# Kernel optimization log

Measured on AMD Instinct MI355X. Metric: run time of the kernel, lower is better.

Reference implementation:

```python
import jax, jax.numpy as jnp
import numpy as np

EPS = 1e-3  # keras BatchNormalization default epsilon


def _dwconv_t(y, w):
    # depthwise conv along time (axis 1), SAME padding. y:(B,T,S,G,n), w:(G,n,k)
    k = w.shape[-1]
    T = y.shape[1]
    pl = (k - 1) // 2
    yp = jnp.pad(y, ((0, 0), (pl, k - 1 - pl), (0, 0), (0, 0), (0, 0)))
    return sum(yp[:, j:j + T] * w[..., j] for j in range(k))


def _tc_layer(x, w, b, k3, k5, k7, gamma, beta, mu, var):
    # x:(B,T,S,C); w:(5,G,Cg,nb); b/gamma/beta/mu/var:(5,G,nb); k*:(G,nb,k)
    B, T, S, C = x.shape
    G, nb = w.shape[1], w.shape[-1]
    # global spatial pooling: concat [x, max, mean] along spatial axis -> S+2
    x = jnp.concatenate([x, x.max(axis=2, keepdims=True), x.mean(axis=2, keepdims=True)], axis=2)
    S = S + 2
    xg = x.reshape(B, T, S, G, C // G)
    # 5 grouped 1x1x1 pointwise convs at once
    y = jnp.einsum('btsgc,pgcn->pbtsgn', xg, w) + b[:, None, None, None]
    t0 = y[0]
    t3 = _dwconv_t(y[1], k3)
    t5 = _dwconv_t(y[2], k5)
    t7 = _dwconv_t(y[3], k7)
    # temporal maxpool pool=2 stride=1 SAME (TF pads right)
    t1 = jnp.maximum(y[4], jnp.concatenate([y[4][:, 1:], y[4][:, -1:]], axis=1))
    ts = jnp.stack([t0, t3, t5, t7, t1])  # (5,B,T,S,G,nb)
    scale = gamma[:, None, None, None] / jnp.sqrt(var[:, None, None, None] + EPS)
    ts = (ts - mu[:, None, None, None]) * scale + beta[:, None, None, None]
    # concat branches within each group: (B,T,S,G,5*nb)
    z = jnp.transpose(ts, (1, 2, 3, 4, 0, 5)).reshape(B, T, S, G, 5 * nb)
    z = jax.nn.relu(z)
    # channel shuffle: (G, per) -> (per, G) -> flatten
    z = jnp.swapaxes(z, -1, -2).reshape(B, T, S, G * 5 * nb)
    # MaxPooling3D pool=(2,1,1) stride 2 valid: halve T
    return jnp.maximum(z[:, 0::2], z[:, 1::2])


def setup_inputs() -> dict:
    key = jax.random.key(0)
    ks = jax.random.split(key, 32)
    B, T, H, W, C = 16, 64, 7, 7, 1024
    G = 8
    d = {'x': jax.random.normal(ks[0], (B, T, H, W, C), jnp.float32)}
    specs = [(0, 128, 32), (1, 160, 40)]  # (layer, Cg, nb)
    i = 1
    for l, cg, nb in specs:
        d[f'w{l}'] = 0.02 * jax.random.normal(ks[i], (5, G, cg, nb)); i += 1
        d[f'b{l}'] = 0.02 * jax.random.normal(ks[i], (5, G, nb)); i += 1
        d[f'k3_{l}'] = 0.1 * jax.random.normal(ks[i], (G, nb, 3)); i += 1
        d[f'k5_{l}'] = 0.1 * jax.random.normal(ks[i], (G, nb, 5)); i += 1
        d[f'k7_{l}'] = 0.1 * jax.random.normal(ks[i], (G, nb, 7)); i += 1
        d[f'g{l}'] = jax.random.uniform(ks[i], (5, G, nb), minval=0.5, maxval=1.5); i += 1
        d[f'be{l}'] = 0.02 * jax.random.normal(ks[i], (5, G, nb)); i += 1
        d[f'mu{l}'] = 0.02 * jax.random.normal(ks[i], (5, G, nb)); i += 1
        d[f'v{l}'] = jax.random.uniform(ks[i], (5, G, nb), minval=0.5, maxval=1.5); i += 1
    return d


def reference(x, w0, b0, k3_0, k5_0, k7_0, g0, be0, mu0, v0,
              w1, b1, k3_1, k5_1, k7_1, g1, be1, mu1, v1):
    B, T, H, W, C = x.shape
    z = x.reshape(B, T, H * W, C)  # (B,T,S,C), side_dim2=1 kept implicit
    z = _tc_layer(z, w0, b0, k3_0, k5_0, k7_0, g0, be0, mu0, v0)
    z = _tc_layer(z, w1, b1, k3_1, k5_1, k7_1, g1, be1, mu1, v1)
    return z[:, :, :, None, :]  # (B, T/4, S+4, 1, Cout)
```

## Files before the change

kernel.cpp:

```cpp
#include <hip/hip_runtime.h>
#include <hip/hip_bf16.h>

#define EPSBN 1e-3f

typedef __attribute__((ext_vector_type(8))) short bf16x8;
typedef __attribute__((ext_vector_type(8))) unsigned short ushort8;
typedef __attribute__((ext_vector_type(4))) float f32x4;


__device__ __forceinline__ float bf2f(unsigned short u) {
    union { unsigned int i; float f; } c; c.i = (unsigned int)u << 16; return c.f;
}
__device__ __forceinline__ unsigned short f2bf(float f) {
    union { float f; unsigned int i; } c; c.f = f;
    unsigned int r = c.i + 0x7FFF + ((c.i >> 16) & 1);
    return (unsigned short)(r >> 16);
}

__global__ __launch_bounds__(256) void tc_prep(const float* __restrict__ w0,
                                               const float* __restrict__ w1,
                                               unsigned short* __restrict__ W0t,
                                               unsigned short* __restrict__ W1t) {
    const int idx = blockIdx.x * 256 + threadIdx.x;
    if (idx < 163840) {
        const int g   = idx / 20480;
        const int rem = idx - g*20480;
        const int n   = rem >> 7;
        const int k   = rem & 127;
        const int p   = n >> 5, nn = n & 31;
        W0t[idx] = f2bf(w0[(((size_t)p*8 + g)*128 + k)*32 + nn]);
    } else if (idx < 163840 + 256000) {
        const int i2  = idx - 163840;
        const int g   = i2 / 32000;
        const int rem = i2 - g*32000;
        const int n   = rem / 160;
        const int k   = rem - n*160;
        const int kref = (k % 20)*8 + k/20;
        const int p   = n / 40, nn = n - p*40;
        W1t[i2] = f2bf(w1[(((size_t)p*8 + g)*160 + kref)*40 + nn]);
    }
}

__global__ __launch_bounds__(256) void tc_reduce0(const float* __restrict__ x,
                                                  unsigned short* __restrict__ xb,
                                                  unsigned short* __restrict__ extb,
                                                  const int big) {
    const int bt = blockIdx.x;
    const int b  = bt >> 6, t = bt & 63;
    const int c  = threadIdx.x * 4;
    const float4* src = reinterpret_cast<const float4*>(x + (size_t)bt * 49 * 1024 + c);
    float4 v = src[0];
    float mx0 = v.x, mx1 = v.y, mx2 = v.z, mx3 = v.w;
    float sm0 = v.x, sm1 = v.y, sm2 = v.z, sm3 = v.w;
    if (big) {
        ushort4 o; o.x=f2bf(v.x); o.y=f2bf(v.y); o.z=f2bf(v.z); o.w=f2bf(v.w);
        *reinterpret_cast<ushort4*>(&xb[((size_t)(b*51)*64 + t)*1024 + c]) = o;
    }
    for (int s = 1; s < 49; ++s) {
        float4 u = src[(size_t)s * 256];
        mx0 = fmaxf(mx0, u.x); sm0 += u.x;
        mx1 = fmaxf(mx1, u.y); sm1 += u.y;
        mx2 = fmaxf(mx2, u.z); sm2 += u.z;
        mx3 = fmaxf(mx3, u.w); sm3 += u.w;
        if (big) {
            ushort4 o; o.x=f2bf(u.x); o.y=f2bf(u.y); o.z=f2bf(u.z); o.w=f2bf(u.w);
            *reinterpret_cast<ushort4*>(&xb[((size_t)(b*51 + s)*64 + t)*1024 + c]) = o;
        }
    }
    const float inv = 1.0f / 49.0f;
    ushort4 omx, omn;
    omx.x=f2bf(mx0); omx.y=f2bf(mx1); omx.z=f2bf(mx2); omx.w=f2bf(mx3);
    omn.x=f2bf(sm0*inv); omn.y=f2bf(sm1*inv); omn.z=f2bf(sm2*inv); omn.w=f2bf(sm3*inv);
    if (big) {
        *reinterpret_cast<ushort4*>(&xb[((size_t)(b*51 + 49)*64 + t)*1024 + c]) = omx;
        *reinterpret_cast<ushort4*>(&xb[((size_t)(b*51 + 50)*64 + t)*1024 + c]) = omn;
    } else {
        *reinterpret_cast<ushort4*>(&extb[((size_t)(b*2 + 0)*64 + t)*1024 + c]) = omx;
        *reinterpret_cast<ushort4*>(&extb[((size_t)(b*2 + 1)*64 + t)*1024 + c]) = omn;
    }
}

template<int BIG>
__global__ __launch_bounds__(256, 5) void tc_layer0(
    const float* __restrict__ x, const unsigned short* __restrict__ xb,
    const unsigned short* __restrict__ extb,
    const unsigned short* __restrict__ W0t, const float* __restrict__ bias,
    const float* __restrict__ k3, const float* __restrict__ k5,
    const float* __restrict__ k7,
    const float* __restrict__ gam, const float* __restrict__ bet,
    const float* __restrict__ mu, const float* __restrict__ var,
    unsigned short* __restrict__ zb)
{
    const int tid = threadIdx.x;
    const int g  = blockIdx.x / 816;
    const int bs = blockIdx.x % 816;
    const int s  = bs % 51;
    const int b  = bs / 51;

    __shared__ __align__(16) unsigned short lds[15104];
    unsigned short* AtU = lds;
    unsigned short* WtU = lds + 64*136;
    unsigned short* Ytb = lds;

    #pragma unroll
    for (int it = 0; it < 4; ++it) {
        const int fid = tid + it*256;
        const int row = fid >> 4;
        const int ch8 = (fid & 15) * 8;
        ushort8 u;
        if (BIG) {
            u = *reinterpret_cast<const ushort8*>(
                &xb[((size_t)(b*51 + s)*64 + row)*1024 + g*128 + ch8]);
        } else if (s < 49) {
            const float* sp = x + ((size_t)(b*64 + row)*49 + s)*1024 + g*128 + ch8;
            const float4 f0 = *reinterpret_cast<const float4*>(sp);
            const float4 f1 = *reinterpret_cast<const float4*>(sp + 4);
            u[0]=f2bf(f0.x); u[1]=f2bf(f0.y); u[2]=f2bf(f0.z); u[3]=f2bf(f0.w);
            u[4]=f2bf(f1.x); u[5]=f2bf(f1.y); u[6]=f2bf(f1.z); u[7]=f2bf(f1.w);
        } else {
            u = *reinterpret_cast<const ushort8*>(
                &extb[((size_t)(b*2 + (s-49))*64 + row)*1024 + g*128 + ch8]);
        }
        *reinterpret_cast<ushort8*>(&AtU[row*136 + ch8]) = u;
    }

    const int lane = tid & 63;
    const int wid  = tid >> 6;
    const int fr   = lane & 15;
    const int kb   = lane >> 4;

    f32x4 zero = {0.f, 0.f, 0.f, 0.f};
    f32x4 acc[10];
    #pragma unroll
    for (int i = 0; i < 10; ++i) acc[i] = zero;

    for (int kc = 0; kc < 4; ++kc) {
        __syncthreads();
        #pragma unroll
        for (int it = 0; it < 3; ++it) {
            const int gi = tid + it*256;
            if (gi < 640) {
                const int n = gi >> 2, part = (gi & 3) * 8;
                *reinterpret_cast<ushort8*>(&WtU[n*40 + part]) =
                    *reinterpret_cast<const ushort8*>(
                        &W0t[((size_t)g*160 + n)*128 + kc*32 + part]);
            }
        }
        __syncthreads();
        const bf16x8 bfrag = *reinterpret_cast<const bf16x8*>(
            &AtU[(wid*16 + fr)*136 + kc*32 + kb*8]);
        #pragma unroll
        for (int nt = 0; nt < 10; ++nt) {
            const bf16x8 afrag = *reinterpret_cast<const bf16x8*>(
                &WtU[(nt*16 + fr)*40 + kb*8]);
            acc[nt] = __builtin_amdgcn_mfma_f32_16x16x32_bf16(afrag, bfrag, acc[nt], 0, 0, 0);
        }
    }
    __syncthreads();
    #pragma unroll
    for (int nt = 0; nt < 10; ++nt)
        #pragma unroll
        for (int r = 0; r < 4; ++r)
            Ytb[(nt*16 + kb*4 + r)*72 + wid*16 + fr] = f2bf(acc[nt][r]);
    __syncthreads();

    if (tid < 160) {
        const int ch = tid;
        const int p  = ch >> 5, n = ch & 31;
        const int pi = (p*8 + g)*32 + n;
        const float bsv = bias[pi];
        const float sc  = gam[pi]*rsqrtf(var[pi]+EPSBN);
        const float sh  = bet[pi] - mu[pi]*sc;
        float yv[64];
        #pragma unroll
        for (int i = 0; i < 8; ++i) {
            const ushort8 u = *reinterpret_cast<const ushort8*>(&Ytb[ch*72 + i*8]);
            #pragma unroll
            for (int j = 0; j < 8; ++j) yv[i*8+j] = bf2f(u[j]) + bsv;
        }
        unsigned short* zp = zb + ((size_t)(b*32)*53 + s)*1280 + g*160 + ch;
        if (p == 0) {
            #pragma unroll
            for (int tq = 0; tq < 32; ++tq) {
                const float r = fmaxf(fmaxf(fmaf(yv[2*tq],sc,sh), fmaf(yv[2*tq+1],sc,sh)), 0.f);
                zp[(size_t)tq*67840] = f2bf(r);
            }
        } else if (p == 1) {
            const float w0_ = k3[(g*32+n)*3+0], w1_ = k3[(g*32+n)*3+1], w2_ = k3[(g*32+n)*3+2];
            #pragma unroll
            for (int tq = 0; tq < 32; ++tq) {
                float a = yv[2*tq]*w1_;
                if (tq > 0) a = fmaf(yv[2*tq-1], w0_, a);
                a = fmaf(yv[2*tq+1], w2_, a);
                float c2 = fmaf(yv[2*tq], w0_, yv[2*tq+1]*w1_);
                if (tq < 31) c2 = fmaf(yv[2*tq+2], w2_, c2);
                const float r = fmaxf(fmaxf(fmaf(a,sc,sh), fmaf(c2,sc,sh)), 0.f);
                zp[(size_t)tq*67840] = f2bf(r);
            }
        } else if (p == 2) {
            float wk[5];
            #pragma unroll
            for (int j = 0; j < 5; ++j) wk[j] = k5[(g*32+n)*5+j];
            #pragma unroll
            for (int tq = 0; tq < 32; ++tq) {
                float vv[2];
                #pragma unroll
                for (int q = 0; q < 2; ++q) {
                    const int t = 2*tq + q;
                    float v = 0.f;
                    #pragma unroll
                    for (int j = 0; j < 5; ++j) {
                        const int ttp = t + j - 2;
                        if (ttp >= 0 && ttp < 64) v = fmaf(yv[ttp], wk[j], v);
                    }
                    vv[q] = v;
                }
                const float r = fmaxf(fmaxf(fmaf(vv[0],sc,sh), fmaf(vv[1],sc,sh)), 0.f);
                zp[(size_t)tq*67840] = f2bf(r);
            }
        } else if (p == 3) {
            float wk[7];
            #pragma unroll
            for (int j = 0; j < 7; ++j) wk[j] = k7[(g*32+n)*7+j];
            #pragma unroll
            for (int tq = 0; tq < 32; ++tq) {
                float vv[2];
                #pragma unroll
                for (int q = 0; q < 2; ++q) {
                    const int t = 2*tq + q;
                    float v = 0.f;
                    #pragma unroll
                    for (int j = 0; j < 7; ++j) {
                        const int ttp = t + j - 3;
                        if (ttp >= 0 && ttp < 64) v = fmaf(yv[ttp], wk[j], v);
                    }
                    vv[q] = v;
                }
                const float r = fmaxf(fmaxf(fmaf(vv[0],sc,sh), fmaf(vv[1],sc,sh)), 0.f);
                zp[(size_t)tq*67840] = f2bf(r);
            }
        } else {
            #pragma unroll
            for (int tq = 0; tq < 32; ++tq) {
                const float v0 = fmaxf(yv[2*tq], yv[2*tq+1]);
                const float v1 = fmaxf(yv[2*tq+1], yv[(2*tq+2 < 64) ? 2*tq+2 : 63]);
                const float r = fmaxf(fmaxf(fmaf(v0,sc,sh), fmaf(v1,sc,sh)), 0.f);
                zp[(size_t)tq*67840] = f2bf(r);
            }
        }
    }
}

__global__ __launch_bounds__(320) void tc_reduce1(unsigned short* __restrict__ zb) {
    const int bt = blockIdx.x;
    const int c  = threadIdx.x * 4;
    unsigned short* base = zb + (size_t)bt * 67840;
    ushort4 u = *reinterpret_cast<const ushort4*>(&base[c]);
    float v0 = bf2f(u.x), v1 = bf2f(u.y), v2 = bf2f(u.z), v3 = bf2f(u.w);
    float mx0 = v0, mx1 = v1, mx2 = v2, mx3 = v3;
    float sm0 = v0, sm1 = v1, sm2 = v2, sm3 = v3;
    for (int s = 1; s < 51; ++s) {
        ushort4 w = *reinterpret_cast<const ushort4*>(&base[(size_t)s*1280 + c]);
        v0 = bf2f(w.x); v1 = bf2f(w.y); v2 = bf2f(w.z); v3 = bf2f(w.w);
        mx0 = fmaxf(mx0, v0); sm0 += v0;
        mx1 = fmaxf(mx1, v1); sm1 += v1;
        mx2 = fmaxf(mx2, v2); sm2 += v2;
        mx3 = fmaxf(mx3, v3); sm3 += v3;
    }
    const float inv = 1.0f / 51.0f;
    ushort4 o;
    o.x = f2bf(mx0); o.y = f2bf(mx1); o.z = f2bf(mx2); o.w = f2bf(mx3);
    *reinterpret_cast<ushort4*>(&base[(size_t)51*1280 + c]) = o;
    o.x = f2bf(sm0*inv); o.y = f2bf(sm1*inv); o.z = f2bf(sm2*inv); o.w = f2bf(sm3*inv);
    *reinterpret_cast<ushort4*>(&base[(size_t)52*1280 + c]) = o;
}

__global__ __launch_bounds__(256, 6) void tc_layer1(
    const unsigned short* __restrict__ zbi,
    const unsigned short* __restrict__ W1t, const float* __restrict__ bias,
    const float* __restrict__ k3, const float* __restrict__ k5,
    const float* __restrict__ k7,
    const float* __restrict__ gam, const float* __restrict__ bet,
    const float* __restrict__ mu, const float* __restrict__ var,
    float* __restrict__ out)
{
    const int tid = threadIdx.x;
    const int g  = blockIdx.x / 848;
    const int bs = blockIdx.x % 848;
    const int s  = bs % 53;
    const int b  = bs / 53;

    __shared__ __align__(16) unsigned short lds[13376];
    unsigned short* AtU = lds;
    unsigned short* WtU = lds + 32*168;
    unsigned short* Ytb = lds;

    #pragma unroll
    for (int it = 0; it < 5; ++it) {
        const int fid = tid + it*256;
        const int t   = fid / 40;
        const int seg = fid - t*40;
        const int gg  = seg / 5, q = seg - gg*5;
        const int ch  = gg*160 + g*20 + q*4;
        const unsigned short* src = zbi + ((size_t)(b*32 + t)*53 + s)*1280 + ch;
        *reinterpret_cast<ushort4*>(&AtU[t*168 + seg*4]) =
            *reinterpret_cast<const ushort4*>(src);
    }

    const int lane = tid & 63;
    const int wid  = tid >> 6;
    const int tt_  = wid & 1;
    const int nh   = wid >> 1;
    const int nbase = nh * 7;
    const int fr   = lane & 15;
    const int kb   = lane >> 4;

    f32x4 zero = {0.f, 0.f, 0.f, 0.f};
    f32x4 acc[7];
    #pragma unroll
    for (int i = 0; i < 7; ++i) acc[i] = zero;

    for (int kc = 0; kc < 5; ++kc) {
        __syncthreads();
        #pragma unroll
        for (int it = 0; it < 4; ++it) {
            const int gi = tid + it*256;
            if (gi < 800) {
                const int n = gi >> 2, part = (gi & 3) * 8;
                *reinterpret_cast<ushort8*>(&WtU[n*40 + part]) =
                    *reinterpret_cast<const ushort8*>(
                        &W1t[((size_t)g*200 + n)*160 + kc*32 + part]);
            }
        }
        __syncthreads();
        const bf16x8 bfrag = *reinterpret_cast<const bf16x8*>(
            &AtU[(tt_*16 + fr)*168 + kc*32 + kb*8]);
        #pragma unroll
        for (int i = 0; i < 7; ++i) {
            const int nt = nbase + i;
            if (nt < 13) {
                const bf16x8 afrag = *reinterpret_cast<const bf16x8*>(
                    &WtU[(nt*16 + fr)*40 + kb*8]);
                acc[i] = __builtin_amdgcn_mfma_f32_16x16x32_bf16(afrag, bfrag, acc[i], 0, 0, 0);
            }
        }
    }
    __syncthreads();
    #pragma unroll
    for (int i = 0; i < 7; ++i) {
        const int nt = nbase + i;
        if (nt < 13) {
            #pragma unroll
            for (int r = 0; r < 4; ++r) {
                const int row = nt*16 + kb*4 + r;
                if (row < 200) Ytb[row*40 + tt_*16 + fr] = f2bf(acc[i][r]);
            }
        }
    }
    __syncthreads();

    if (tid < 200) {
        const int ch = tid;
        const int p  = ch / 40, n = ch - p*40;
        const int pi = (p*8 + g)*40 + n;
        const float bsv = bias[pi];
        const float sc  = gam[pi]*rsqrtf(var[pi]+EPSBN);
        const float sh  = bet[pi] - mu[pi]*sc;
        float yv[32];
        #pragma unroll
        for (int i = 0; i < 4; ++i) {
            const ushort8 u = *reinterpret_cast<const ushort8*>(&Ytb[ch*40 + i*8]);
            #pragma unroll
            for (int j = 0; j < 8; ++j) yv[i*8+j] = bf2f(u[j]) + bsv;
        }
        float* op = out + ((size_t)(b*16)*53 + s)*1600 + g*200 + ch;
        if (p == 0) {
            #pragma unroll
            for (int tq = 0; tq < 16; ++tq)
                op[(size_t)tq*84800] =
                    fmaxf(fmaxf(fmaf(yv[2*tq],sc,sh), fmaf(yv[2*tq+1],sc,sh)), 0.f);
        } else if (p == 1) {
            const float w0_ = k3[(g*40+n)*3+0], w1_ = k3[(g*40+n)*3+1], w2_ = k3[(g*40+n)*3+2];
            #pragma unroll
            for (int tq = 0; tq < 16; ++tq) {
                float a = yv[2*tq]*w1_;
                if (tq > 0) a = fmaf(yv[2*tq-1], w0_, a);
                a = fmaf(yv[2*tq+1], w2_, a);
                float c2 = fmaf(yv[2*tq], w0_, yv[2*tq+1]*w1_);
                if (tq < 15) c2 = fmaf(yv[2*tq+2], w2_, c2);
                op[(size_t)tq*84800] = fmaxf(fmaxf(fmaf(a,sc,sh), fmaf(c2,sc,sh)), 0.f);
            }
        } else if (p == 2) {
            float wk[5];
            #pragma unroll
            for (int j = 0; j < 5; ++j) wk[j] = k5[(g*40+n)*5+j];
            #pragma unroll
            for (int tq = 0; tq < 16; ++tq) {
                float vv[2];
                #pragma unroll
                for (int q = 0; q < 2; ++q) {
                    const int t = 2*tq + q;
                    float v = 0.f;
                    #pragma unroll
                    for (int j = 0; j < 5; ++j) {
                        const int ttp = t + j - 2;
                        if (ttp >= 0 && ttp < 32) v = fmaf(yv[ttp], wk[j], v);
                    }
                    vv[q] = v;
                }
                op[(size_t)tq*84800] = fmaxf(fmaxf(fmaf(vv[0],sc,sh), fmaf(vv[1],sc,sh)), 0.f);
            }
        } else if (p == 3) {
            float wk[7];
            #pragma unroll
            for (int j = 0; j < 7; ++j) wk[j] = k7[(g*40+n)*7+j];
            #pragma unroll
            for (int tq = 0; tq < 16; ++tq) {
                float vv[2];
                #pragma unroll
                for (int q = 0; q < 2; ++q) {
                    const int t = 2*tq + q;
                    float v = 0.f;
                    #pragma unroll
                    for (int j = 0; j < 7; ++j) {
                        const int ttp = t + j - 3;
                        if (ttp >= 0 && ttp < 32) v = fmaf(yv[ttp], wk[j], v);
                    }
                    vv[q] = v;
                }
                op[(size_t)tq*84800] = fmaxf(fmaxf(fmaf(vv[0],sc,sh), fmaf(vv[1],sc,sh)), 0.f);
            }
        } else {
            #pragma unroll
            for (int tq = 0; tq < 16; ++tq) {
                const float v0 = fmaxf(yv[2*tq], yv[2*tq+1]);
                const float v1 = fmaxf(yv[2*tq+1], yv[(2*tq+2 < 32) ? 2*tq+2 : 31]);
                op[(size_t)tq*84800] = fmaxf(fmaxf(fmaf(v0,sc,sh), fmaf(v1,sc,sh)), 0.f);
            }
        }
    }
}

__global__ __launch_bounds__(256) void tc_shuffle(float* __restrict__ o) {
    __shared__ float row[1600];
    const size_t base = (size_t)blockIdx.x * 1600;
    const int tid = threadIdx.x;
    #pragma unroll
    for (int it = 0; it < 2; ++it) {
        const int f4 = tid + it*256;
        if (f4 < 400)
            *reinterpret_cast<float4*>(&row[f4*4]) =
                *reinterpret_cast<const float4*>(&o[base + (size_t)f4*4]);
    }
    __syncthreads();
    #pragma unroll
    for (int it = 0; it < 2; ++it) {
        const int f4 = tid + it*256;
        if (f4 < 400) {
            const int c = f4*4;
            float4 v;
            v.x = row[((c  ) & 7)*200 + ((c  ) >> 3)];
            v.y = row[((c+1) & 7)*200 + ((c+1) >> 3)];
            v.z = row[((c+2) & 7)*200 + ((c+2) >> 3)];
            v.w = row[((c+3) & 7)*200 + ((c+3) >> 3)];
            *reinterpret_cast<float4*>(&o[base + (size_t)c]) = v;
        }
    }
}

extern "C" void kernel_launch(void* const* d_in, const int* in_sizes, int n_in,
                              void* d_out, int out_size, void* d_ws, size_t ws_size,
                              hipStream_t stream) {
    const float* x    = (const float*)d_in[0];
    const float* w0   = (const float*)d_in[1];
    const float* b0   = (const float*)d_in[2];
    const float* k3_0 = (const float*)d_in[3];
    const float* k5_0 = (const float*)d_in[4];
    const float* k7_0 = (const float*)d_in[5];
    const float* g0   = (const float*)d_in[6];
    const float* be0  = (const float*)d_in[7];
    const float* mu0  = (const float*)d_in[8];
    const float* v0   = (const float*)d_in[9];
    const float* w1   = (const float*)d_in[10];
    const float* b1   = (const float*)d_in[11];
    const float* k3_1 = (const float*)d_in[12];
    const float* k5_1 = (const float*)d_in[13];
    const float* k7_1 = (const float*)d_in[14];
    const float* g1   = (const float*)d_in[15];
    const float* be1  = (const float*)d_in[16];
    const float* mu1  = (const float*)d_in[17];
    const float* v1   = (const float*)d_in[18];

    const size_t n_zb   = 34734080;
    const size_t n_W0t  = 163840;
    const size_t n_W1t  = 256000;
    const size_t n_extb = 2097152;
    const size_t n_xb   = 53477376;

    unsigned short* zb   = (unsigned short*)d_ws;
    unsigned short* W0t  = zb + n_zb;
    unsigned short* W1t  = W0t + n_W0t;
    unsigned short* extb = W1t + n_W1t;
    unsigned short* xb   = extb + n_extb;
    const size_t need_big = (n_zb + n_W0t + n_W1t + n_extb + n_xb) * 2;
    const int big = (ws_size >= need_big) ? 1 : 0;

    tc_prep   <<<1640, 256, 0, stream>>>(w0, w1, W0t, W1t);
    tc_reduce0<<<16*64, 256, 0, stream>>>(x, xb, extb, big);
    if (big)
        tc_layer0<1><<<816*8, 256, 0, stream>>>(x, xb, extb, W0t, b0, k3_0, k5_0,
                                                k7_0, g0, be0, mu0, v0, zb);
    else
        tc_layer0<0><<<816*8, 256, 0, stream>>>(x, xb, extb, W0t, b0, k3_0, k5_0,
                                                k7_0, g0, be0, mu0, v0, zb);
    tc_reduce1<<<16*32, 320, 0, stream>>>(zb);
    tc_layer1 <<<848*8, 256, 0, stream>>>(zb, W1t, b1, k3_1, k5_1, k7_1,
                                          g1, be1, mu1, v1, (float*)d_out);
    tc_shuffle<<<16*16*53, 256, 0, stream>>>((float*)d_out);
}
```

Measured before the change: 286.6 us.

## Process two spatial positions per layer1 block and stage output in bf16

Layer1 blocks now cover two spatial positions, 64 time rows, so each block loads its weight tiles once for twice the work, with each wave computing all 13 N-tiles. The layer1 intermediate is written as bf16 to a new workspace buffer and converted to fp32 in the shuffle kernel, which halves scatter-write and reread traffic. The LDS row stride drops from 72 to 70 in layer0 and is 70 in layer1, read with 32-bit loads, to reduce bank conflicts. The cost is more accumulator registers, lower occupancy (launch bound 4), an extra bf16 rounding of the output, and a larger workspace requirement.

```diff
diff --git a/kernel.cpp b/kernel.cpp
--- a/kernel.cpp
+++ b/kernel.cpp
@@ -161,7 +161,7 @@
     for (int nt = 0; nt < 10; ++nt)
         #pragma unroll
         for (int r = 0; r < 4; ++r)
-            Ytb[(nt*16 + kb*4 + r)*72 + wid*16 + fr] = f2bf(acc[nt][r]);
+            Ytb[(nt*16 + kb*4 + r)*70 + wid*16 + fr] = f2bf(acc[nt][r]);
     __syncthreads();
 
     if (tid < 160) {
@@ -173,10 +173,10 @@
         const float sh  = bet[pi] - mu[pi]*sc;
         float yv[64];
         #pragma unroll
-        for (int i = 0; i < 8; ++i) {
-            const ushort8 u = *reinterpret_cast<const ushort8*>(&Ytb[ch*72 + i*8]);
-            #pragma unroll
-            for (int j = 0; j < 8; ++j) yv[i*8+j] = bf2f(u[j]) + bsv;
+        for (int i = 0; i < 32; ++i) {
+            const unsigned int w2 = *reinterpret_cast<const unsigned int*>(&Ytb[ch*70 + i*2]);
+            yv[2*i]   = bf2f((unsigned short)(w2 & 0xffffu)) + bsv;
+            yv[2*i+1] = bf2f((unsigned short)(w2 >> 16)) + bsv;
         }
         unsigned short* zp = zb + ((size_t)(b*32)*53 + s)*1280 + g*160 + ch;
         if (p == 0) {
@@ -275,50 +275,57 @@
     *reinterpret_cast<ushort4*>(&base[(size_t)52*1280 + c]) = o;
 }
 
-__global__ __launch_bounds__(256, 6) void tc_layer1(
+__global__ __launch_bounds__(256, 4) void tc_layer1(
     const unsigned short* __restrict__ zbi,
     const unsigned short* __restrict__ W1t, const float* __restrict__ bias,
     const float* __restrict__ k3, const float* __restrict__ k5,
     const float* __restrict__ k7,
     const float* __restrict__ gam, const float* __restrict__ bet,
     const float* __restrict__ mu, const float* __restrict__ var,
-    float* __restrict__ out)
+    unsigned short* __restrict__ og)
 {
     const int tid = threadIdx.x;
-    const int g  = blockIdx.x / 848;
-    const int bs = blockIdx.x % 848;
-    const int s  = bs % 53;
-    const int b  = bs / 53;
-
-    __shared__ __align__(16) unsigned short lds[13376];
+    const int g   = blockIdx.x / 432;
+    const int rem = blockIdx.x % 432;
+    const int sp  = rem % 27;
+    const int b   = rem / 27;
+    const int s0  = sp*2;
+    const int has1 = (s0 + 1 < 53);
+
+    __shared__ __align__(16) unsigned short lds[64*168 + 208*40];
     unsigned short* AtU = lds;
-    unsigned short* WtU = lds + 32*168;
+    unsigned short* WtU = lds + 64*168;
     unsigned short* Ytb = lds;
 
-    #pragma unroll
-    for (int it = 0; it < 5; ++it) {
+    if (tid < 40) {
+        ushort8 z8 = {0,0,0,0,0,0,0,0};
+        const int r = tid / 5, cp = tid - r*5;
+        *reinterpret_cast<ushort8*>(&WtU[(200 + r)*40 + cp*8]) = z8;
+    }
+
+    #pragma unroll
+    for (int it = 0; it < 10; ++it) {
         const int fid = tid + it*256;
-        const int t   = fid / 40;
-        const int seg = fid - t*40;
+        const int row = fid / 40;
+        const int seg = fid - row*40;
         const int gg  = seg / 5, q = seg - gg*5;
         const int ch  = gg*160 + g*20 + q*4;
+        const int s   = (row < 32) ? s0 : (has1 ? s0+1 : s0);
+        const int t   = row & 31;
         const unsigned short* src = zbi + ((size_t)(b*32 + t)*53 + s)*1280 + ch;
-        *reinterpret_cast<ushort4*>(&AtU[t*168 + seg*4]) =
+        *reinterpret_cast<ushort4*>(&AtU[row*168 + seg*4]) =
             *reinterpret_cast<const ushort4*>(src);
     }
 
     const int lane = tid & 63;
     const int wid  = tid >> 6;
-    const int tt_  = wid & 1;
-    const int nh   = wid >> 1;
-    const int nbase = nh * 7;
     const int fr   = lane & 15;
     const int kb   = lane >> 4;
 
     f32x4 zero = {0.f, 0.f, 0.f, 0.f};
-    f32x4 acc[7];
-    #pragma unroll
-    for (int i = 0; i < 7; ++i) acc[i] = zero;
+    f32x4 acc[13];
+    #pragma unroll
+    for (int i = 0; i < 13; ++i) acc[i] = zero;
 
     for (int kc = 0; kc < 5; ++kc) {
         __syncthreads();
@@ -334,124 +341,128 @@
         }
         __syncthreads();
         const bf16x8 bfrag = *reinterpret_cast<const bf16x8*>(
-            &AtU[(tt_*16 + fr)*168 + kc*32 + kb*8]);
-        #pragma unroll
-        for (int i = 0; i < 7; ++i) {
-            const int nt = nbase + i;
-            if (nt < 13) {
-                const bf16x8 afrag = *reinterpret_cast<const bf16x8*>(
-                    &WtU[(nt*16 + fr)*40 + kb*8]);
-                acc[i] = __builtin_amdgcn_mfma_f32_16x16x32_bf16(afrag, bfrag, acc[i], 0, 0, 0);
-            }
+            &AtU[(wid*16 + fr)*168 + kc*32 + kb*8]);
+        #pragma unroll
+        for (int nt = 0; nt < 13; ++nt) {
+            const bf16x8 afrag = *reinterpret_cast<const bf16x8*>(
+                &WtU[(nt*16 + fr)*40 + kb*8]);
+            acc[nt] = __builtin_amdgcn_mfma_f32_16x16x32_bf16(afrag, bfrag, acc[nt], 0, 0, 0);
         }
     }
     __syncthreads();
     #pragma unroll
-    for (int i = 0; i < 7; ++i) {
-        const int nt = nbase + i;
-        if (nt < 13) {
-            #pragma unroll
-            for (int r = 0; r < 4; ++r) {
-                const int row = nt*16 + kb*4 + r;
-                if (row < 200) Ytb[row*40 + tt_*16 + fr] = f2bf(acc[i][r]);
-            }
+    for (int nt = 0; nt < 13; ++nt) {
+        #pragma unroll
+        for (int r = 0; r < 4; ++r) {
+            const int n = nt*16 + kb*4 + r;
+            if (n < 200) Ytb[n*70 + wid*16 + fr] = f2bf(acc[nt][r]);
         }
     }
     __syncthreads();
 
-    if (tid < 200) {
-        const int ch = tid;
-        const int p  = ch / 40, n = ch - p*40;
-        const int pi = (p*8 + g)*40 + n;
-        const float bsv = bias[pi];
-        const float sc  = gam[pi]*rsqrtf(var[pi]+EPSBN);
-        const float sh  = bet[pi] - mu[pi]*sc;
-        float yv[32];
-        #pragma unroll
-        for (int i = 0; i < 4; ++i) {
-            const ushort8 u = *reinterpret_cast<const ushort8*>(&Ytb[ch*40 + i*8]);
-            #pragma unroll
-            for (int j = 0; j < 8; ++j) yv[i*8+j] = bf2f(u[j]) + bsv;
-        }
-        float* op = out + ((size_t)(b*16)*53 + s)*1600 + g*200 + ch;
-        if (p == 0) {
-            #pragma unroll
-            for (int tq = 0; tq < 16; ++tq)
-                op[(size_t)tq*84800] =
-                    fmaxf(fmaxf(fmaf(yv[2*tq],sc,sh), fmaf(yv[2*tq+1],sc,sh)), 0.f);
-        } else if (p == 1) {
-            const float w0_ = k3[(g*40+n)*3+0], w1_ = k3[(g*40+n)*3+1], w2_ = k3[(g*40+n)*3+2];
-            #pragma unroll
-            for (int tq = 0; tq < 16; ++tq) {
-                float a = yv[2*tq]*w1_;
-                if (tq > 0) a = fmaf(yv[2*tq-1], w0_, a);
-                a = fmaf(yv[2*tq+1], w2_, a);
-                float c2 = fmaf(yv[2*tq], w0_, yv[2*tq+1]*w1_);
-                if (tq < 15) c2 = fmaf(yv[2*tq+2], w2_, c2);
-                op[(size_t)tq*84800] = fmaxf(fmaxf(fmaf(a,sc,sh), fmaf(c2,sc,sh)), 0.f);
-            }
-        } else if (p == 2) {
-            float wk[5];
-            #pragma unroll
-            for (int j = 0; j < 5; ++j) wk[j] = k5[(g*40+n)*5+j];
-            #pragma unroll
-            for (int tq = 0; tq < 16; ++tq) {
-                float vv[2];
-                #pragma unroll
-                for (int q = 0; q < 2; ++q) {
-                    const int t = 2*tq + q;
-                    float v = 0.f;
+    #pragma unroll
+    for (int it = 0; it < 2; ++it) {
+        const int task = tid + it*256;
+        if (task < 400) {
+            const int sIdx = (task >= 200) ? 1 : 0;
+            const int ch   = task - sIdx*200;
+            if (sIdx && !has1) continue;
+            const int s  = s0 + sIdx;
+            const int p  = ch / 40, n = ch - p*40;
+            const int pi = (p*8 + g)*40 + n;
+            const float bsv = bias[pi];
+            const float sc  = gam[pi]*rsqrtf(var[pi]+EPSBN);
+            const float sh  = bet[pi] - mu[pi]*sc;
+            float yv[32];
+            #pragma unroll
+            for (int i = 0; i < 16; ++i) {
+                const unsigned int w2 = *reinterpret_cast<const unsigned int*>(
+                    &Ytb[ch*70 + sIdx*32 + i*2]);
+                yv[2*i]   = bf2f((unsigned short)(w2 & 0xffffu)) + bsv;
+                yv[2*i+1] = bf2f((unsigned short)(w2 >> 16)) + bsv;
+            }
+            unsigned short* op = og + ((size_t)(b*16)*53 + s)*1600 + g*200 + ch;
+            if (p == 0) {
+                #pragma unroll
+                for (int tq = 0; tq < 16; ++tq) {
+                    const float r = fmaxf(fmaxf(fmaf(yv[2*tq],sc,sh), fmaf(yv[2*tq+1],sc,sh)), 0.f);
+                    op[(size_t)tq*84800] = f2bf(r);
+                }
+            } else if (p == 1) {
+                const float w0_ = k3[(g*40+n)*3+0], w1_ = k3[(g*40+n)*3+1], w2_ = k3[(g*40+n)*3+2];
+                #pragma unroll
+                for (int tq = 0; tq < 16; ++tq) {
+                    float a = yv[2*tq]*w1_;
+                    if (tq > 0) a = fmaf(yv[2*tq-1], w0_, a);
+                    a = fmaf(yv[2*tq+1], w2_, a);
+                    float c2 = fmaf(yv[2*tq], w0_, yv[2*tq+1]*w1_);
+                    if (tq < 15) c2 = fmaf(yv[2*tq+2], w2_, c2);
+                    const float r = fmaxf(fmaxf(fmaf(a,sc,sh), fmaf(c2,sc,sh)), 0.f);
+                    op[(size_t)tq*84800] = f2bf(r);
+                }
+            } else if (p == 2) {
+                float wk[5];
+                #pragma unroll
+                for (int j = 0; j < 5; ++j) wk[j] = k5[(g*40+n)*5+j];
+                #pragma unroll
+                for (int tq = 0; tq < 16; ++tq) {
+                    float vv[2];
                     #pragma unroll
-                    for (int j = 0; j < 5; ++j) {
-                        const int ttp = t + j - 2;
-                        if (ttp >= 0 && ttp < 32) v = fmaf(yv[ttp], wk[j], v);
+                    for (int q = 0; q < 2; ++q) {
+                        const int t = 2*tq + q;
+                        float v = 0.f;
+                        #pragma unroll
+                        for (int j = 0; j < 5; ++j) {
+                            const int ttp = t + j - 2;
+                            if (ttp >= 0 && ttp < 32) v = fmaf(yv[ttp], wk[j], v);
+                        }
+                        vv[q] = v;
                     }
-                    vv[q] = v;
-                }
-                op[(size_t)tq*84800] = fmaxf(fmaxf(fmaf(vv[0],sc,sh), fmaf(vv[1],sc,sh)), 0.f);
-            }
-        } else if (p == 3) {
-            float wk[7];
-            #pragma unroll
-            for (int j = 0; j < 7; ++j) wk[j] = k7[(g*40+n)*7+j];
-            #pragma unroll
-            for (int tq = 0; tq < 16; ++tq) {
-                float vv[2];
-                #pragma unroll
-                for (int q = 0; q < 2; ++q) {
-                    const int t = 2*tq + q;
-                    float v = 0.f;
+                    const float r = fmaxf(fmaxf(fmaf(vv[0],sc,sh), fmaf(vv[1],sc,sh)), 0.f);
+                    op[(size_t)tq*84800] = f2bf(r);
+                }
+            } else if (p == 3) {
+                float wk[7];
+                #pragma unroll
+                for (int j = 0; j < 7; ++j) wk[j] = k7[(g*40+n)*7+j];
+                #pragma unroll
+                for (int tq = 0; tq < 16; ++tq) {
+                    float vv[2];
                     #pragma unroll
-                    for (int j = 0; j < 7; ++j) {
-                        const int ttp = t + j - 3;
-                        if (ttp >= 0 && ttp < 32) v = fmaf(yv[ttp], wk[j], v);
+                    for (int q = 0; q < 2; ++q) {
+                        const int t = 2*tq + q;
+                        float v = 0.f;
+                        #pragma unroll
+                        for (int j = 0; j < 7; ++j) {
+                            const int ttp = t + j - 3;
+                            if (ttp >= 0 && ttp < 32) v = fmaf(yv[ttp], wk[j], v);
+                        }
+                        vv[q] = v;
                     }
-                    vv[q] = v;
-                }
-                op[(size_t)tq*84800] = fmaxf(fmaxf(fmaf(vv[0],sc,sh), fmaf(vv[1],sc,sh)), 0.f);
-            }
-        } else {
-            #pragma unroll
-            for (int tq = 0; tq < 16; ++tq) {
-                const float v0 = fmaxf(yv[2*tq], yv[2*tq+1]);
-                const float v1 = fmaxf(yv[2*tq+1], yv[(2*tq+2 < 32) ? 2*tq+2 : 31]);
-                op[(size_t)tq*84800] = fmaxf(fmaxf(fmaf(v0,sc,sh), fmaf(v1,sc,sh)), 0.f);
-            }
-        }
-    }
-}
-
-__global__ __launch_bounds__(256) void tc_shuffle(float* __restrict__ o) {
-    __shared__ float row[1600];
+                    const float r = fmaxf(fmaxf(fmaf(vv[0],sc,sh), fmaf(vv[1],sc,sh)), 0.f);
+                    op[(size_t)tq*84800] = f2bf(r);
+                }
+            } else {
+                #pragma unroll
+                for (int tq = 0; tq < 16; ++tq) {
+                    const float v0 = fmaxf(yv[2*tq], yv[2*tq+1]);
+                    const float v1 = fmaxf(yv[2*tq+1], yv[(2*tq+2 < 32) ? 2*tq+2 : 31]);
+                    const float r = fmaxf(fmaxf(fmaf(v0,sc,sh), fmaf(v1,sc,sh)), 0.f);
+                    op[(size_t)tq*84800] = f2bf(r);
+                }
+            }
+        }
+    }
+}
+
+__global__ __launch_bounds__(256) void tc_shuffle(const unsigned short* __restrict__ og,
+                                                  float* __restrict__ o) {
+    __shared__ unsigned short row[1600];
     const size_t base = (size_t)blockIdx.x * 1600;
     const int tid = threadIdx.x;
-    #pragma unroll
-    for (int it = 0; it < 2; ++it) {
-        const int f4 = tid + it*256;
-        if (f4 < 400)
-            *reinterpret_cast<float4*>(&row[f4*4]) =
-                *reinterpret_cast<const float4*>(&o[base + (size_t)f4*4]);
-    }
+    if (tid < 200)
+        *reinterpret_cast<ushort8*>(&row[tid*8]) =
+            *reinterpret_cast<const ushort8*>(&og[base + (size_t)tid*8]);
     __syncthreads();
     #pragma unroll
     for (int it = 0; it < 2; ++it) {
@@ -459,10 +470,10 @@
         if (f4 < 400) {
             const int c = f4*4;
             float4 v;
-            v.x = row[((c  ) & 7)*200 + ((c  ) >> 3)];
-            v.y = row[((c+1) & 7)*200 + ((c+1) >> 3)];
-            v.z = row[((c+2) & 7)*200 + ((c+2) >> 3)];
-            v.w = row[((c+3) & 7)*200 + ((c+3) >> 3)];
+            v.x = bf2f(row[((c  ) & 7)*200 + ((c  ) >> 3)]);
+            v.y = bf2f(row[((c+1) & 7)*200 + ((c+1) >> 3)]);
+            v.z = bf2f(row[((c+2) & 7)*200 + ((c+2) >> 3)]);
+            v.w = bf2f(row[((c+3) & 7)*200 + ((c+3) >> 3)]);
             *reinterpret_cast<float4*>(&o[base + (size_t)c]) = v;
         }
     }
@@ -495,14 +506,16 @@
     const size_t n_W0t  = 163840;
     const size_t n_W1t  = 256000;
     const size_t n_extb = 2097152;
+    const size_t n_og   = 21708800;
     const size_t n_xb   = 53477376;
 
     unsigned short* zb   = (unsigned short*)d_ws;
     unsigned short* W0t  = zb + n_zb;
     unsigned short* W1t  = W0t + n_W0t;
     unsigned short* extb = W1t + n_W1t;
-    unsigned short* xb   = extb + n_extb;
-    const size_t need_big = (n_zb + n_W0t + n_W1t + n_extb + n_xb) * 2;
+    unsigned short* og   = extb + n_extb;
+    unsigned short* xb   = og + n_og;
+    const size_t need_big = (n_zb + n_W0t + n_W1t + n_extb + n_og + n_xb) * 2;
     const int big = (ws_size >= need_big) ? 1 : 0;
 
     tc_prep   <<<1640, 256, 0, stream>>>(w0, w1, W0t, W1t);
@@ -514,7 +527,7 @@
         tc_layer0<0><<<816*8, 256, 0, stream>>>(x, xb, extb, W0t, b0, k3_0, k5_0,
                                                 k7_0, g0, be0, mu0, v0, zb);
     tc_reduce1<<<16*32, 320, 0, stream>>>(zb);
-    tc_layer1 <<<848*8, 256, 0, stream>>>(zb, W1t, b1, k3_1, k5_1, k7_1,
-                                          g1, be1, mu1, v1, (float*)d_out);
-    tc_shuffle<<<16*16*53, 256, 0, stream>>>((float*)d_out);
-}
+    tc_layer1 <<<432*8, 256, 0, stream>>>(zb, W1t, b1, k3_1, k5_1, k7_1,
+                                          g1, be1, mu1, v1, og);
+    tc_shuffle<<<16*16*53, 256, 0, stream>>>(og, (float*)d_out);
+}
```

Measured after the change: 265.1 us. 1.08x faster.
